# Kernel tuning notes

Hardware: AMD Instinct MI355X
Metric: run time of the kernel (lower is better)

## Reference

```python
import jax, jax.numpy as jnp
import numpy as np

N_NODES = 100000


def _gcn_conv(x, edge_index, W, b, num_nodes):
    """PyG GCNConv: x' = D^{-1/2} (A + I) D^{-1/2} (x W) + b."""
    xl = x @ W  # [N, H]
    loop = jnp.arange(num_nodes)
    row = jnp.concatenate([edge_index[0], loop])  # source
    col = jnp.concatenate([edge_index[1], loop])  # target
    deg = jax.ops.segment_sum(jnp.ones_like(col, dtype=xl.dtype), col,
                              num_segments=num_nodes)
    dinv = jnp.where(deg > 0, jax.lax.rsqrt(deg), 0.0)
    norm = dinv[row] * dinv[col]  # [E + N]
    msgs = xl[row] * norm[:, None]  # gather + scale
    out = jax.ops.segment_sum(msgs, col, num_segments=num_nodes)
    return out + b


def setup_inputs() -> dict:
    key = jax.random.key(0)
    ks = jax.random.split(key, 6)
    N, E, D, H, O = N_NODES, 1600000, 128, 64, 1
    x = jax.random.normal(ks[0], (N, D), dtype=jnp.float32)
    edge_index = jax.random.randint(ks[1], (2, E), 0, N, dtype=jnp.int64)
    W1 = jax.random.normal(ks[2], (D, H), dtype=jnp.float32) / np.sqrt(D)
    b1 = jnp.zeros((H,), dtype=jnp.float32)
    W2 = jax.random.normal(ks[3], (H, H), dtype=jnp.float32) / np.sqrt(H)
    b2 = jnp.zeros((H,), dtype=jnp.float32)
    Wfc = jax.random.normal(ks[4], (H, O), dtype=jnp.float32) / np.sqrt(H)
    bfc = jnp.zeros((O,), dtype=jnp.float32)
    return {"x": x, "edge_index": edge_index, "W1": W1, "b1": b1,
            "W2": W2, "b2": b2, "Wfc": Wfc, "bfc": bfc}


def reference(x, edge_index, W1, b1, W2, b2, Wfc, bfc):
    N = x.shape[0]
    h = jax.nn.relu(_gcn_conv(x, edge_index, W1, b1, N))
    h = jax.nn.relu(_gcn_conv(h, edge_index, W2, b2, N))
    return jax.nn.sigmoid(h @ Wfc + bfc)  # [N, 1]
```

## Files before the change

### kernel.cpp

```cpp
#include <hip/hip_runtime.h>
#include <math.h>


typedef __attribute__((ext_vector_type(8))) short bf16x8;
typedef __attribute__((ext_vector_type(4))) float f32x4;
typedef __attribute__((ext_vector_type(2))) float f32x2;

#define CHUNKS 1024

__device__ __forceinline__ unsigned short f2bf(float f) {
    unsigned u = __float_as_uint(f);
    u += 0x7FFFu + ((u >> 16) & 1u);
    return (unsigned short)(u >> 16);
}
__device__ __forceinline__ unsigned packbf(float a, float b) {
    return (unsigned)f2bf(a) | ((unsigned)f2bf(b) << 16);
}
__device__ __forceinline__ void upadd2(uint4 g, f32x2* a) {
    a[0] += (f32x2){__uint_as_float(g.x << 16), __uint_as_float(g.x & 0xFFFF0000u)};
    a[1] += (f32x2){__uint_as_float(g.y << 16), __uint_as_float(g.y & 0xFFFF0000u)};
    a[2] += (f32x2){__uint_as_float(g.z << 16), __uint_as_float(g.z & 0xFFFF0000u)};
    a[3] += (f32x2){__uint_as_float(g.w << 16), __uint_as_float(g.w & 0xFFFF0000u)};
}


__global__ __launch_bounds__(256) void k_hist(const int* __restrict__ col, int E,
                                              int NBUK, int CH,
                                              int* __restrict__ hist_g) {
    __shared__ int h[256];
    for (int i = threadIdx.x; i < NBUK; i += 256) h[i] = 0;
    __syncthreads();
    int base = blockIdx.x * CH, hi = min(base + CH, E);
    for (int e = base + (int)threadIdx.x; e < hi; e += 256)
        atomicAdd(&h[col[e] >> 9], 1);
    __syncthreads();
    for (int i = threadIdx.x; i < NBUK; i += 256)
        hist_g[blockIdx.x * NBUK + i] = h[i];
}

__global__ __launch_bounds__(256) void k_colscan(const int* __restrict__ hist_g, int NBUK,
                                                 int* __restrict__ histOff,
                                                 int* __restrict__ bucketTotal) {
    __shared__ int s[256];
    const int b = blockIdx.x, t = threadIdx.x;
    int v[4], sum = 0;
#pragma unroll
    for (int j = 0; j < 4; ++j) {
        v[j] = hist_g[(t * 4 + j) * NBUK + b];
        sum += v[j];
    }
    s[t] = sum;
    __syncthreads();
    for (int off = 1; off < 256; off <<= 1) {
        int u = (t >= off) ? s[t - off] : 0;
        __syncthreads();
        s[t] += u;
        __syncthreads();
    }
    int run = s[t] - sum;
#pragma unroll
    for (int j = 0; j < 4; ++j) {
        histOff[b * CHUNKS + t * 4 + j] = run;
        run += v[j];
    }
    if (t == 255) bucketTotal[b] = run;
}

__global__ __launch_bounds__(256) void k_scan_tot(const int* __restrict__ bucketTotal,
                                                  int NBUK, int E, int N,
                                                  int* __restrict__ bucketBase,
                                                  int* __restrict__ row_off) {
    __shared__ int s[256];
    int t = threadIdx.x;
    int v = (t < NBUK) ? bucketTotal[t] : 0;
    s[t] = v;
    __syncthreads();
    for (int off = 1; off < 256; off <<= 1) {
        int u = (t >= off) ? s[t - off] : 0;
        __syncthreads();
        s[t] += u;
        __syncthreads();
    }
    if (t < NBUK) bucketBase[t] = s[t] - v;
    if (t == 0) row_off[N] = E;
}

__global__ __launch_bounds__(256) void k_scatter(const int* __restrict__ row,
                                                 const int* __restrict__ col, int E,
                                                 int NBUK, int CH,
                                                 const int* __restrict__ bucketBase,
                                                 const int* __restrict__ histOff,
                                                 unsigned* __restrict__ ebuf) {
    __shared__ int cur[256];
    for (int i = threadIdx.x; i < NBUK; i += 256)
        cur[i] = bucketBase[i] + histOff[i * CHUNKS + blockIdx.x];
    __syncthreads();
    int base = blockIdx.x * CH, hi = min(base + CH, E);
    for (int e = base + (int)threadIdx.x; e < hi; e += 256) {
        int d = col[e], src = row[e];
        int b = d >> 9;
        int pos = atomicAdd(&cur[b], 1);
        ebuf[pos] = ((unsigned)(d & 511) << 17) | (unsigned)src;
    }
}

__global__ __launch_bounds__(512) void k_bucket(const unsigned* __restrict__ ebuf,
                                                const int* __restrict__ bucketBase,
                                                const int* __restrict__ bucketTotal,
                                                int N,
                                                int* __restrict__ row_off,
                                                float* __restrict__ dinv,
                                                int* __restrict__ csr_src) {
    __shared__ int hc[512], of[512];
    const int bid = blockIdx.x, t = threadIdx.x;
    const int base = bucketBase[bid];
    const int cnt  = bucketTotal[bid];
    hc[t] = 0;
    __syncthreads();
    for (int i = t; i < cnt; i += 512)
        atomicAdd(&hc[ebuf[base + i] >> 17], 1);
    __syncthreads();
    int v = hc[t];
    of[t] = v;
    __syncthreads();
    for (int off = 1; off < 512; off <<= 1) {
        int u = (t >= off) ? of[t - off] : 0;
        __syncthreads();
        of[t] += u;
        __syncthreads();
    }
    int excl = of[t] - v;
    int node = bid * 512 + t;
    if (node < N) {
        row_off[node] = base + excl;
        dinv[node] = rsqrtf((float)(v + 1));
    }
    of[t] = excl;
    __syncthreads();
    for (int i = t; i < cnt; i += 512) {
        unsigned e = ebuf[base + i];
        int dl = (int)(e >> 17), src = (int)(e & 0x1FFFFu);
        int pos = atomicAdd(&of[dl], 1);
        csr_src[base + pos] = src;
    }
}

template <int K, bool BF16IN>
__global__ __launch_bounds__(256) void k_gemm_mfma(const void* __restrict__ xin,
                                                   const float* __restrict__ W,
                                                   const float* __restrict__ dinv,
                                                   unsigned short* __restrict__ out,
                                                   int N) {
    constexpr int KS = K + 8;
    __shared__ short sX[64 * KS];
    __shared__ short sW[64 * KS];
    const int tid = threadIdx.x;
    const int wv = tid >> 6, lane = tid & 63;
    const int q = lane >> 4, m = lane & 15;
    const int nb = blockIdx.x * 64;

    for (int i = tid; i < K * 64; i += 256) {
        int k = i >> 6, c = i & 63;
        sW[c * KS + k] = (short)f2bf(W[i]);
    }
    if (BF16IN) {
        const unsigned short* xb = (const unsigned short*)xin;
        for (int i = tid; i < 64 * (K / 8); i += 256) {
            int r = i / (K / 8), c8 = (i % (K / 8)) * 8;
            int node = nb + r;
            uint4 v = make_uint4(0u, 0u, 0u, 0u);
            if (node < N) v = *(const uint4*)(xb + (size_t)node * K + c8);
            *(uint4*)(&sX[r * KS + c8]) = v;
        }
    } else {
        const float* xf = (const float*)xin;
        for (int i = tid; i < 64 * (K / 8); i += 256) {
            int r = i / (K / 8), c8 = (i % (K / 8)) * 8;
            int node = nb + r;
            uint4 v = make_uint4(0u, 0u, 0u, 0u);
            if (node < N) {
                float4 lo = *(const float4*)(xf + (size_t)node * K + c8);
                float4 hi = *(const float4*)(xf + (size_t)node * K + c8 + 4);
                v.x = packbf(lo.x, lo.y);
                v.y = packbf(lo.z, lo.w);
                v.z = packbf(hi.x, hi.y);
                v.w = packbf(hi.z, hi.w);
            }
            *(uint4*)(&sX[r * KS + c8]) = v;
        }
    }
    __syncthreads();

    f32x4 acc[4] = {};
    const short* aRow = &sX[(wv * 16 + m) * KS + q * 8];
#pragma unroll
    for (int k0 = 0; k0 < K; k0 += 32) {
        bf16x8 a = *(const bf16x8*)(aRow + k0);
#pragma unroll
        for (int ft = 0; ft < 4; ++ft) {
            bf16x8 b = *(const bf16x8*)(&sW[(ft * 16 + m) * KS + k0 + q * 8]);
            acc[ft] = __builtin_amdgcn_mfma_f32_16x16x32_bf16(a, b, acc[ft], 0, 0, 0);
        }
    }
#pragma unroll
    for (int r = 0; r < 4; ++r) {
        int node = nb + wv * 16 + q * 4 + r;
        if (node < N) {
            float di = dinv[node];
#pragma unroll
            for (int ft = 0; ft < 4; ++ft)
                out[(size_t)node * 64 + ft * 16 + m] = f2bf(acc[ft][r] * di);
        }
    }
}

__global__ __launch_bounds__(256) void k_agg(const unsigned short* __restrict__ xl,
                                             const int* __restrict__ row_off,
                                             const int* __restrict__ csr_src,
                                             const float* __restrict__ dinv,
                                             const float* __restrict__ bias,
                                             unsigned short* __restrict__ out, int N) {
    const int wave = threadIdx.x >> 6, lane = threadIdx.x & 63;
    const int s = lane >> 3, o = lane & 7;
    const int node = blockIdx.x * 4 + wave;
    if (node >= N) return;
    const int beg = row_off[node], end = row_off[node + 1];
    const int em1 = end - 1;
    const char* xlb = (const char*)xl;
    const unsigned loff = (unsigned)(o << 4);
    f32x2 acc[4] = {};
    uint4 selfv = *(const uint4*)(xlb + (((unsigned)node << 7) | loff));
    int idx1 = csr_src[min(beg + s, max(em1, 0))];
    int idx2 = csr_src[min(beg + 8 + s, max(em1, 0))];
    for (int base = beg; base < end; base += 16) {
        const int c1 = idx1, c2 = idx2;
        const bool v1 = (base + s) < end, v2 = (base + 8 + s) < end;
        idx1 = csr_src[min(base + 16 + s, em1)];
        idx2 = csr_src[min(base + 24 + s, em1)];
        uint4 g1 = *(const uint4*)(xlb + (((unsigned)c1 << 7) | loff));
        uint4 g2 = *(const uint4*)(xlb + (((unsigned)c2 << 7) | loff));
        if (!v1) g1 = make_uint4(0u, 0u, 0u, 0u);
        if (!v2) g2 = make_uint4(0u, 0u, 0u, 0u);
        upadd2(g1, acc);
        upadd2(g2, acc);
    }
#pragma unroll
    for (int m = 8; m <= 32; m <<= 1)
#pragma unroll
        for (int j = 0; j < 4; ++j) {
            acc[j].x += __shfl_xor(acc[j].x, m, 64);
            acc[j].y += __shfl_xor(acc[j].y, m, 64);
        }
    upadd2(selfv, acc);
    if (s == 0) {
        float di = dinv[node];
        float4 blo = *(const float4*)(bias + o * 8);
        float4 bhi = *(const float4*)(bias + o * 8 + 4);
        uint4 r;
        r.x = packbf(fmaxf(acc[0].x * di + blo.x, 0.f), fmaxf(acc[0].y * di + blo.y, 0.f));
        r.y = packbf(fmaxf(acc[1].x * di + blo.z, 0.f), fmaxf(acc[1].y * di + blo.w, 0.f));
        r.z = packbf(fmaxf(acc[2].x * di + bhi.x, 0.f), fmaxf(acc[2].y * di + bhi.y, 0.f));
        r.w = packbf(fmaxf(acc[3].x * di + bhi.z, 0.f), fmaxf(acc[3].y * di + bhi.w, 0.f));
        *(uint4*)(out + (size_t)node * 64 + o * 8) = r;
    }
}

__global__ __launch_bounds__(256) void k_agg_fc(const unsigned short* __restrict__ xl,
                                                const int* __restrict__ row_off,
                                                const int* __restrict__ csr_src,
                                                const float* __restrict__ dinv,
                                                const float* __restrict__ bias,
                                                const float* __restrict__ Wfc,
                                                const float* __restrict__ bfc,
                                                float* __restrict__ out, int N) {
    const int wave = threadIdx.x >> 6, lane = threadIdx.x & 63;
    const int s = lane >> 3, o = lane & 7;
    const int node = blockIdx.x * 4 + wave;
    if (node >= N) return;
    const int beg = row_off[node], end = row_off[node + 1];
    const int em1 = end - 1;
    const char* xlb = (const char*)xl;
    const unsigned loff = (unsigned)(o << 4);
    f32x2 acc[4] = {};
    uint4 selfv = *(const uint4*)(xlb + (((unsigned)node << 7) | loff));
    int idx1 = csr_src[min(beg + s, max(em1, 0))];
    int idx2 = csr_src[min(beg + 8 + s, max(em1, 0))];
    for (int base = beg; base < end; base += 16) {
        const int c1 = idx1, c2 = idx2;
        const bool v1 = (base + s) < end, v2 = (base + 8 + s) < end;
        idx1 = csr_src[min(base + 16 + s, em1)];
        idx2 = csr_src[min(base + 24 + s, em1)];
        uint4 g1 = *(const uint4*)(xlb + (((unsigned)c1 << 7) | loff));
        uint4 g2 = *(const uint4*)(xlb + (((unsigned)c2 << 7) | loff));
        if (!v1) g1 = make_uint4(0u, 0u, 0u, 0u);
        if (!v2) g2 = make_uint4(0u, 0u, 0u, 0u);
        upadd2(g1, acc);
        upadd2(g2, acc);
    }
#pragma unroll
    for (int m = 8; m <= 32; m <<= 1)
#pragma unroll
        for (int j = 0; j < 4; ++j) {
            acc[j].x += __shfl_xor(acc[j].x, m, 64);
            acc[j].y += __shfl_xor(acc[j].y, m, 64);
        }
    upadd2(selfv, acc);
    const float di = dinv[node];
    float4 blo = *(const float4*)(bias + o * 8);
    float4 bhi = *(const float4*)(bias + o * 8 + 4);
    float4 wlo = *(const float4*)(Wfc + o * 8);
    float4 whi = *(const float4*)(Wfc + o * 8 + 4);
    float v = 0.f;
    v += fmaxf(acc[0].x * di + blo.x, 0.f) * wlo.x;
    v += fmaxf(acc[0].y * di + blo.y, 0.f) * wlo.y;
    v += fmaxf(acc[1].x * di + blo.z, 0.f) * wlo.z;
    v += fmaxf(acc[1].y * di + blo.w, 0.f) * wlo.w;
    v += fmaxf(acc[2].x * di + bhi.x, 0.f) * whi.x;
    v += fmaxf(acc[2].y * di + bhi.y, 0.f) * whi.y;
    v += fmaxf(acc[3].x * di + bhi.z, 0.f) * whi.z;
    v += fmaxf(acc[3].y * di + bhi.w, 0.f) * whi.w;
#pragma unroll
    for (int m = 1; m <= 4; m <<= 1) v += __shfl_xor(v, m, 64);
    if (lane == 0) out[node] = 1.f / (1.f + expf(-(v + bfc[0])));
}

extern "C" void kernel_launch(void* const* d_in, const int* in_sizes, int n_in,
                              void* d_out, int out_size, void* d_ws, size_t ws_size,
                              hipStream_t stream) {
    const float* x   = (const float*)d_in[0];
    const int*   ei  = (const int*)d_in[1];
    const float* W1  = (const float*)d_in[2];
    const float* b1  = (const float*)d_in[3];
    const float* W2  = (const float*)d_in[4];
    const float* b2  = (const float*)d_in[5];
    const float* Wfc = (const float*)d_in[6];
    const float* bfc = (const float*)d_in[7];
    float* out = (float*)d_out;

    const int H = in_sizes[3];
    const int D = in_sizes[2] / H;
    const int N = in_sizes[0] / D;
    const int E = in_sizes[1] / 2;
    const int* row = ei;
    const int* col = ei + E;
    const int NBUK = (N + 511) >> 9;
    const int CH   = (E + CHUNKS - 1) / CHUNKS;

    char* p = (char*)d_ws;
    auto carve = [&](size_t bytes) {
        char* r = p;
        p += (bytes + 255) & ~(size_t)255;
        return (void*)r;
    };
    int*            hist_g      = (int*)carve((size_t)CHUNKS * 256 * 4);
    int*            histOff     = (int*)carve((size_t)256 * CHUNKS * 4);
    int*            bucketTotal = (int*)carve((size_t)256 * 4);
    int*            bucketBase  = (int*)carve((size_t)256 * 4);
    unsigned*       ebuf        = (unsigned*)carve((size_t)E * 4);
    int*            csr_src     = (int*)carve((size_t)E * 4);
    int*            row_off     = (int*)carve((size_t)(N + 1) * 4);
    float*          dinv        = (float*)carve((size_t)N * 4);
    unsigned short* bufXL       = (unsigned short*)carve((size_t)N * 64 * 2);
    unsigned short* bufH        = (unsigned short*)carve((size_t)N * 64 * 2);
    (void)ws_size;

    const int TB = 256;
    k_hist<<<CHUNKS, TB, 0, stream>>>(col, E, NBUK, CH, hist_g);
    k_colscan<<<NBUK, TB, 0, stream>>>(hist_g, NBUK, histOff, bucketTotal);
    k_scan_tot<<<1, TB, 0, stream>>>(bucketTotal, NBUK, E, N, bucketBase, row_off);
    k_scatter<<<CHUNKS, TB, 0, stream>>>(row, col, E, NBUK, CH, bucketBase, histOff, ebuf);
    k_bucket<<<NBUK, 512, 0, stream>>>(ebuf, bucketBase, bucketTotal, N,
                                       row_off, dinv, csr_src);

    int gemmGrid = (N + 63) / 64;
    int aggGrid  = (N + 3) / 4;
    k_gemm_mfma<128, false><<<gemmGrid, TB, 0, stream>>>(x, W1, dinv, bufXL, N);
    k_agg<<<aggGrid, TB, 0, stream>>>(bufXL, row_off, csr_src, dinv, b1, bufH, N);
    k_gemm_mfma<64, true><<<gemmGrid, TB, 0, stream>>>(bufH, W2, dinv, bufXL, N);
    k_agg_fc<<<aggGrid, TB, 0, stream>>>(bufXL, row_off, csr_src, dinv, b2, Wfc, bfc, out, N);
}
```

Measured before the change: 237.4 us.

## Map eight nodes per wave in aggregation kernels instead of one

The two aggregation kernels now give each 8-lane group its own destination node, so a wave handles eight nodes and walks each node's edges serially, instead of one node per wave split across eight edge slots. The cross-group shuffle reduction goes away, the self-loop is folded into the loop as an extra iteration, and the grid shrinks eightfold. The aim is to remove per-node reduction overhead and wasted lanes on the small average degree (about 16). The cost is that each wave loops to the maximum degree among its eight nodes, and there is less memory-level parallelism per node because only one gather per group is in flight per iteration.

```diff
diff --git a/kernel.cpp b/kernel.cpp
--- a/kernel.cpp
+++ b/kernel.cpp
@@ -22,7 +22,6 @@
     a[2] += (f32x2){__uint_as_float(g.z << 16), __uint_as_float(g.z & 0xFFFF0000u)};
     a[3] += (f32x2){__uint_as_float(g.w << 16), __uint_as_float(g.w & 0xFFFF0000u)};
 }
-
 
 __global__ __launch_bounds__(256) void k_hist(const int* __restrict__ col, int E,
                                               int NBUK, int CH,
@@ -222,37 +221,30 @@
                                              unsigned short* __restrict__ out, int N) {
     const int wave = threadIdx.x >> 6, lane = threadIdx.x & 63;
     const int s = lane >> 3, o = lane & 7;
-    const int node = blockIdx.x * 4 + wave;
-    if (node >= N) return;
-    const int beg = row_off[node], end = row_off[node + 1];
-    const int em1 = end - 1;
+    int node = (blockIdx.x * 4 + wave) * 8 + s;
+    const bool active = node < N;
+    node = min(node, N - 1);
+    const int beg = row_off[node];
+    const int deg = row_off[node + 1] - beg;
+    const int cnt = active ? deg + 1 : 0;
+    int mx = cnt;
+    mx = max(mx, __shfl_xor(mx, 8, 64));
+    mx = max(mx, __shfl_xor(mx, 16, 64));
+    mx = max(mx, __shfl_xor(mx, 32, 64));
     const char* xlb = (const char*)xl;
     const unsigned loff = (unsigned)(o << 4);
     f32x2 acc[4] = {};
-    uint4 selfv = *(const uint4*)(xlb + (((unsigned)node << 7) | loff));
-    int idx1 = csr_src[min(beg + s, max(em1, 0))];
-    int idx2 = csr_src[min(beg + 8 + s, max(em1, 0))];
-    for (int base = beg; base < end; base += 16) {
-        const int c1 = idx1, c2 = idx2;
-        const bool v1 = (base + s) < end, v2 = (base + 8 + s) < end;
-        idx1 = csr_src[min(base + 16 + s, em1)];
-        idx2 = csr_src[min(base + 24 + s, em1)];
-        uint4 g1 = *(const uint4*)(xlb + (((unsigned)c1 << 7) | loff));
-        uint4 g2 = *(const uint4*)(xlb + (((unsigned)c2 << 7) | loff));
-        if (!v1) g1 = make_uint4(0u, 0u, 0u, 0u);
-        if (!v2) g2 = make_uint4(0u, 0u, 0u, 0u);
-        upadd2(g1, acc);
-        upadd2(g2, acc);
-    }
-#pragma unroll
-    for (int m = 8; m <= 32; m <<= 1)
-#pragma unroll
-        for (int j = 0; j < 4; ++j) {
-            acc[j].x += __shfl_xor(acc[j].x, m, 64);
-            acc[j].y += __shfl_xor(acc[j].y, m, 64);
-        }
-    upadd2(selfv, acc);
-    if (s == 0) {
+    int idx = (0 < deg) ? csr_src[beg] : node;
+    for (int it = 0; it < mx; ++it) {
+        const int cur = idx;
+        const bool valid = it < cnt;
+        const int nit = it + 1;
+        idx = (nit < deg) ? csr_src[beg + nit] : node;
+        uint4 g = *(const uint4*)(xlb + (((unsigned)cur << 7) | loff));
+        if (!valid) g = make_uint4(0u, 0u, 0u, 0u);
+        upadd2(g, acc);
+    }
+    if (active) {
         float di = dinv[node];
         float4 blo = *(const float4*)(bias + o * 8);
         float4 bhi = *(const float4*)(bias + o * 8 + 4);
@@ -275,36 +267,29 @@
                                                 float* __restrict__ out, int N) {
     const int wave = threadIdx.x >> 6, lane = threadIdx.x & 63;
     const int s = lane >> 3, o = lane & 7;
-    const int node = blockIdx.x * 4 + wave;
-    if (node >= N) return;
-    const int beg = row_off[node], end = row_off[node + 1];
-    const int em1 = end - 1;
+    int node = (blockIdx.x * 4 + wave) * 8 + s;
+    const bool active = node < N;
+    node = min(node, N - 1);
+    const int beg = row_off[node];
+    const int deg = row_off[node + 1] - beg;
+    const int cnt = active ? deg + 1 : 0;
+    int mx = cnt;
+    mx = max(mx, __shfl_xor(mx, 8, 64));
+    mx = max(mx, __shfl_xor(mx, 16, 64));
+    mx = max(mx, __shfl_xor(mx, 32, 64));
     const char* xlb = (const char*)xl;
     const unsigned loff = (unsigned)(o << 4);
     f32x2 acc[4] = {};
-    uint4 selfv = *(const uint4*)(xlb + (((unsigned)node << 7) | loff));
-    int idx1 = csr_src[min(beg + s, max(em1, 0))];
-    int idx2 = csr_src[min(beg + 8 + s, max(em1, 0))];
-    for (int base = beg; base < end; base += 16) {
-        const int c1 = idx1, c2 = idx2;
-        const bool v1 = (base + s) < end, v2 = (base + 8 + s) < end;
-        idx1 = csr_src[min(base + 16 + s, em1)];
-        idx2 = csr_src[min(base + 24 + s, em1)];
-        uint4 g1 = *(const uint4*)(xlb + (((unsigned)c1 << 7) | loff));
-        uint4 g2 = *(const uint4*)(xlb + (((unsigned)c2 << 7) | loff));
-        if (!v1) g1 = make_uint4(0u, 0u, 0u, 0u);
-        if (!v2) g2 = make_uint4(0u, 0u, 0u, 0u);
-        upadd2(g1, acc);
-        upadd2(g2, acc);
-    }
-#pragma unroll
-    for (int m = 8; m <= 32; m <<= 1)
-#pragma unroll
-        for (int j = 0; j < 4; ++j) {
-            acc[j].x += __shfl_xor(acc[j].x, m, 64);
-            acc[j].y += __shfl_xor(acc[j].y, m, 64);
-        }
-    upadd2(selfv, acc);
+    int idx = (0 < deg) ? csr_src[beg] : node;
+    for (int it = 0; it < mx; ++it) {
+        const int cur = idx;
+        const bool valid = it < cnt;
+        const int nit = it + 1;
+        idx = (nit < deg) ? csr_src[beg + nit] : node;
+        uint4 g = *(const uint4*)(xlb + (((unsigned)cur << 7) | loff));
+        if (!valid) g = make_uint4(0u, 0u, 0u, 0u);
+        upadd2(g, acc);
+    }
     const float di = dinv[node];
     float4 blo = *(const float4*)(bias + o * 8);
     float4 bhi = *(const float4*)(bias + o * 8 + 4);
@@ -319,9 +304,10 @@
     v += fmaxf(acc[2].y * di + bhi.y, 0.f) * whi.y;
     v += fmaxf(acc[3].x * di + bhi.z, 0.f) * whi.z;
     v += fmaxf(acc[3].y * di + bhi.w, 0.f) * whi.w;
-#pragma unroll
-    for (int m = 1; m <= 4; m <<= 1) v += __shfl_xor(v, m, 64);
-    if (lane == 0) out[node] = 1.f / (1.f + expf(-(v + bfc[0])));
+    v += __shfl_xor(v, 1, 64);
+    v += __shfl_xor(v, 2, 64);
+    v += __shfl_xor(v, 4, 64);
+    if (active && o == 0) out[node] = 1.f / (1.f + expf(-(v + bfc[0])));
 }
 
 extern "C" void kernel_launch(void* const* d_in, const int* in_sizes, int n_in,
@@ -373,7 +359,7 @@
                                        row_off, dinv, csr_src);
 
     int gemmGrid = (N + 63) / 64;
-    int aggGrid  = (N + 3) / 4;
+    int aggGrid  = (N + 31) / 32;
     k_gemm_mfma<128, false><<<gemmGrid, TB, 0, stream>>>(x, W1, dinv, bufXL, N);
     k_agg<<<aggGrid, TB, 0, stream>>>(bufXL, row_off, csr_src, dinv, b1, bufH, N);
     k_gemm_mfma<64, true><<<gemmGrid, TB, 0, stream>>>(bufH, W2, dinv, bufXL, N);
```

New measurement: 245.8 us. 3.5% more time.
